# Optimization experiments

Measured on AMD Instinct MI355X. Metric: run time of the kernel, lower is better.

Reference implementation:

```python
import jax, jax.numpy as jnp
import numpy as np

B, S, D, H = 2, 2048, 1024, 16
HD = D // H  # 64
LN_EPS = 1e-5


def setup_inputs() -> dict:
    key = jax.random.key(0)
    ks = jax.random.split(key, 5)
    hidden_states = jax.random.normal(ks[0], (B, S, D), dtype=jnp.float32)
    attention_mask = jnp.zeros((B, 1, 1, S), dtype=jnp.float32)  # additive mask
    # LayerNorm params
    ln_gamma = jnp.ones((D,), dtype=jnp.float32)
    ln_beta = jnp.zeros((D,), dtype=jnp.float32)
    # Q/K/V projections, no bias; stored as [in, out]
    sc = 1.0 / np.sqrt(D)
    Wq = jax.random.normal(ks[1], (D, D), dtype=jnp.float32) * sc
    Wk = jax.random.normal(ks[2], (D, D), dtype=jnp.float32) * sc
    Wv = jax.random.normal(ks[3], (D, D), dtype=jnp.float32) * sc
    return {"hidden_states": hidden_states, "attention_mask": attention_mask,
            "ln_gamma": ln_gamma, "ln_beta": ln_beta, "Wq": Wq, "Wk": Wk, "Wv": Wv}


def _layernorm(x, g, b):
    mu = jnp.mean(x, axis=-1, keepdims=True)
    var = jnp.mean(jnp.square(x - mu), axis=-1, keepdims=True)
    return (x - mu) * jax.lax.rsqrt(var + LN_EPS) * g + b


def reference(hidden_states, attention_mask, ln_gamma, ln_beta, Wq, Wk, Wv):
    h = _layernorm(hidden_states, ln_gamma, ln_beta)          # [B,S,D]
    # project and split heads: [B,S,D] -> [B,H,S,HD]
    def split_heads(x):
        return x.reshape(B, S, H, HD).transpose(0, 2, 1, 3)
    q = split_heads(h @ Wq)
    k = split_heads(h @ Wk)
    v = split_heads(h @ Wv)
    scores = jnp.einsum('bhqd,bhkd->bhqk', q, k) / jnp.sqrt(jnp.float32(HD))
    scores = scores + attention_mask                           # additive mask broadcast
    probs = jax.nn.softmax(scores, axis=-1)                    # dropout p=0 -> identity
    ctx = jnp.einsum('bhqk,bhkd->bhqd', probs, v)              # [B,H,S,HD]
    ctx = ctx.transpose(0, 2, 1, 3).reshape(B, S, H * HD)      # [B,S,D]
    return ctx
```

## Files before the change

kernel.cpp:

```cpp
#include <hip/hip_runtime.h>
#include <hip/hip_bf16.h>
#include <cstdint>

#define B_ 2
#define S_ 2048
#define D_ 1024
#define H_ 16
#define HD_ 64
#define M_ (B_*S_)

#define LOG2E 1.4426950408889634f
#define C1_ (0.125f * LOG2E)

typedef unsigned short u16;
typedef __bf16 bf16x8 __attribute__((ext_vector_type(8)));
typedef u16 u16x8 __attribute__((ext_vector_type(8)));
typedef float f32x4 __attribute__((ext_vector_type(4)));
typedef float f32x16 __attribute__((ext_vector_type(16)));
typedef int i32x4 __attribute__((ext_vector_type(4)));

static __device__ __forceinline__ u16 f2bu(float f) {
  __bf16 b = (__bf16)f;
  return __builtin_bit_cast(unsigned short, b);
}
static __device__ __forceinline__ float bu2f(u16 u) {
  unsigned int v = ((unsigned int)u) << 16;
  return __builtin_bit_cast(float, v);
}

static __device__ __forceinline__ int cvtpk(float a, float b) {
  int r;
  asm("v_cvt_pk_bf16_f32 %0, %1, %2" : "=v"(r) : "v"(a), "v"(b));
  return r;
}
static __device__ __forceinline__ void plswap(int &x, int &y) {
  asm("v_permlane32_swap_b32 %0, %1" : "+v"(x), "+v"(y));
}

#define GLOAD16(g, l) __builtin_amdgcn_global_load_lds( \
    (__attribute__((address_space(1))) void*)(g), \
    (__attribute__((address_space(3))) void*)(l), 16, 0, 0)

__global__ __launch_bounds__(256) void mask_prep(const float* __restrict__ mask,
    float* __restrict__ ms) {
  const int i = blockIdx.x * 256 + threadIdx.x;
  float4 mv = reinterpret_cast<const float4*>(mask)[i];
  float4 sm = {mv.x * LOG2E - 8.0f, mv.y * LOG2E - 8.0f,
               mv.z * LOG2E - 8.0f, mv.w * LOG2E - 8.0f};
  reinterpret_cast<float4*>(ms)[i] = sm;
}

__global__ __launch_bounds__(256) void ln_kernel(const float* __restrict__ x,
    const float* __restrict__ g, const float* __restrict__ be, u16* __restrict__ h) {
  const int row = blockIdx.x;
  const int t = threadIdx.x;
  float4 v = reinterpret_cast<const float4*>(x + (size_t)row * D_)[t];
  float s = v.x + v.y + v.z + v.w;
  float sq = v.x*v.x + v.y*v.y + v.z*v.z + v.w*v.w;
  #pragma unroll
  for (int off = 32; off >= 1; off >>= 1) {
    s  += __shfl_down(s, off);
    sq += __shfl_down(sq, off);
  }
  __shared__ float red[8];
  const int wave = t >> 6, lane = t & 63;
  if (lane == 0) { red[wave] = s; red[4 + wave] = sq; }
  __syncthreads();
  if (t == 0) {
    float ts = red[0]+red[1]+red[2]+red[3];
    float tq = red[4]+red[5]+red[6]+red[7];
    float mu = ts * (1.0f / D_);
    red[0] = mu;
    red[1] = rsqrtf(tq * (1.0f / D_) - mu*mu + 1e-5f);
  }
  __syncthreads();
  const float mu = red[0], rs = red[1];
  float4 gg = reinterpret_cast<const float4*>(g)[t];
  float4 bb = reinterpret_cast<const float4*>(be)[t];
  ushort4 o;
  o.x = f2bu((v.x - mu) * rs * gg.x + bb.x);
  o.y = f2bu((v.y - mu) * rs * gg.y + bb.y);
  o.z = f2bu((v.z - mu) * rs * gg.z + bb.z);
  o.w = f2bu((v.w - mu) * rs * gg.w + bb.w);
  reinterpret_cast<ushort4*>(h + (size_t)row * D_)[t] = o;
}

__global__ __launch_bounds__(256) void wt_kernel(const float* __restrict__ W0,
    const float* __restrict__ W1, const float* __restrict__ W2, u16* __restrict__ wt) {
  const int z = blockIdx.z;
  const float* W = (z == 0) ? W0 : ((z == 1) ? W1 : W2);
  u16* out = wt + (size_t)z * D_ * D_;
  __shared__ float tile[32][33];
  const int n0 = blockIdx.x * 32, k0 = blockIdx.y * 32;
  const int tx = threadIdx.x, ty = threadIdx.y;
  #pragma unroll
  for (int j = 0; j < 4; ++j)
    tile[ty + 8*j][tx] = W[(size_t)(k0 + ty + 8*j) * D_ + n0 + tx];
  __syncthreads();
  #pragma unroll
  for (int j = 0; j < 4; ++j)
    out[(size_t)(n0 + ty + 8*j) * D_ + k0 + tx] = f2bu(tile[tx][ty + 8*j]);
}

__global__ __launch_bounds__(256) void qkv_gemm(const u16* __restrict__ hbuf,
    const u16* __restrict__ wt, u16* __restrict__ qkv) {
  const int z = blockIdx.z;
  const u16* Bt = wt + (size_t)z * D_ * D_;
  u16* outp = qkv + (size_t)z * (B_*H_*S_*HD_);
  __shared__ __align__(16) u16 As[128 * 32];
  __shared__ __align__(16) u16 Bs[128 * 32];
  const int t = threadIdx.x, lane = t & 63, wave = t >> 6;
  const int row0 = blockIdx.y * 128, col0 = blockIdx.x * 128;
  const int wm = wave >> 1, wn = wave & 1;
  f32x4 acc[4][4] = {};
  const int schunk = (t & 3) ^ ((t >> 3) & 3);
  const u16* ag = hbuf + (size_t)(row0 + (t >> 2)) * D_ + schunk * 8;
  const u16* bg = Bt   + (size_t)(col0 + (t >> 2)) * D_ + schunk * 8;
  u16* lA = &As[wave * 512];
  u16* lB = &Bs[wave * 512];
  const char* Ac = (const char*)As;
  const char* Bc = (const char*)Bs;
  const int cbase = (((lane >> 4) ^ ((lane >> 1) & 3)) << 4);

  for (int k0 = 0; k0 < D_; k0 += 32) {
    GLOAD16(ag + k0,           lA);
    GLOAD16(ag + k0 + 64 * D_, lA + 2048);
    GLOAD16(bg + k0,           lB);
    GLOAD16(bg + k0 + 64 * D_, lB + 2048);
    __syncthreads();
    bf16x8 af[4], bfr[4];
    #pragma unroll
    for (int m = 0; m < 4; ++m)
      af[m] = *reinterpret_cast<const bf16x8*>(Ac + (wm*64 + m*16 + (lane & 15)) * 64 + cbase);
    #pragma unroll
    for (int n = 0; n < 4; ++n)
      bfr[n] = *reinterpret_cast<const bf16x8*>(Bc + (wn*64 + n*16 + (lane & 15)) * 64 + cbase);
    #pragma unroll
    for (int m = 0; m < 4; ++m) {
      #pragma unroll
      for (int n = 0; n < 4; ++n)
        acc[m][n] = __builtin_amdgcn_mfma_f32_16x16x32_bf16(af[m], bfr[n], acc[m][n], 0, 0, 0);
    }
    __syncthreads();
  }
  const float scl = (z == 0) ? C1_ : 1.0f;
  #pragma unroll
  for (int m = 0; m < 4; ++m) {
    #pragma unroll
    for (int n = 0; n < 4; ++n) {
      const int gcol = col0 + wn*64 + n*16 + (lane & 15);
      const int hI = gcol >> 6, dI = gcol & 63;
      #pragma unroll
      for (int r = 0; r < 4; ++r) {
        const int grow = row0 + wm*64 + m*16 + (lane >> 4) * 4 + r;
        const int bI = grow >> 11, sI = grow & (S_ - 1);
        size_t idx;
        if (z == 2) idx = ((size_t)(bI * H_ + hI) * HD_ + dI) * S_ + sI;
        else        idx = ((size_t)(bI * H_ + hI) * S_ + sI) * HD_ + dI;
        outp[idx] = f2bu(acc[m][n][r] * scl);
      }
    }
  }
}

static __device__ __forceinline__ void sm_pack(
    const f32x16& s, const float4* __restrict__ mk,
    float& dm, float& lsum, f32x16& o0, f32x16& o1,
    bf16x8& pfA, bf16x8& pfB) {
  float zb[16];
  #pragma unroll
  for (int r = 0; r < 4; ++r) {
    zb[r]      = s[r]      + ((const float*)&mk[0])[r];
    zb[r + 4]  = s[r + 4]  + ((const float*)&mk[1])[r];
    zb[r + 8]  = s[r + 8]  + ((const float*)&mk[2])[r];
    zb[r + 12] = s[r + 12] + ((const float*)&mk[3])[r];
  }
  float a0 = fmaxf(fmaxf(zb[0], zb[1]), zb[2]);
  float a1 = fmaxf(fmaxf(zb[3], zb[4]), zb[5]);
  float a2 = fmaxf(fmaxf(zb[6], zb[7]), zb[8]);
  float a3 = fmaxf(fmaxf(zb[9], zb[10]), zb[11]);
  float a4 = fmaxf(fmaxf(zb[12], zb[13]), zb[14]);
  float tm = fmaxf(fmaxf(fmaxf(a0, a1), fmaxf(a2, a3)), fmaxf(a4, zb[15]));
  if (__builtin_expect(__any(tm > dm + 8.0f), 0)) {
    float tp = fmaxf(tm, __shfl_xor(tm, 32));
    float dnew = fmaxf(dm, tp - 8.0f);
    float sf = __builtin_amdgcn_exp2f(dm - dnew);
    lsum *= sf; o0 = o0 * sf; o1 = o1 * sf; dm = dnew;
  }
  float p[16];
  #pragma unroll
  for (int r = 0; r < 16; ++r) p[r] = __builtin_amdgcn_exp2f(zb[r] - dm);
  float s01 = (p[0] + p[1]) + (p[2] + p[3]);
  float s23 = (p[4] + p[5]) + (p[6] + p[7]);
  float s45 = (p[8] + p[9]) + (p[10] + p[11]);
  float s67 = (p[12] + p[13]) + (p[14] + p[15]);
  lsum += (s01 + s23) + (s45 + s67);
  int pk01 = cvtpk(p[0], p[1]),   pk23 = cvtpk(p[2], p[3]);
  int pk45 = cvtpk(p[4], p[5]),   pk67 = cvtpk(p[6], p[7]);
  int pk89 = cvtpk(p[8], p[9]),   pkAB = cvtpk(p[10], p[11]);
  int pkCD = cvtpk(p[12], p[13]), pkEF = cvtpk(p[14], p[15]);
  plswap(pk01, pk45); plswap(pk23, pk67);
  plswap(pk89, pkCD); plswap(pkAB, pkEF);
  i32x4 c0 = {pk01, pk23, pk45, pk67};
  i32x4 c1 = {pk89, pkAB, pkCD, pkEF};
  pfA = __builtin_bit_cast(bf16x8, c0);
  pfB = __builtin_bit_cast(bf16x8, c1);
}

__global__ __launch_bounds__(256, 3) void attn_kernel(const u16* __restrict__ qkv,
    const float* __restrict__ maskScaled, float* __restrict__ out,
    u16* __restrict__ part1, float* __restrict__ l0a, float* __restrict__ dm0a,
    float* __restrict__ l1a, float* __restrict__ dm1a) {
  const int bid = blockIdx.x;
  const int x = bid & 7, rr = bid >> 3;
  const int w = rr & 31;
  const int pidx = x + ((rr >> 5) << 3);
  const int j = w & 15, g = w >> 4;
  const int hI = pidx & 15, bI = pidx >> 4;
  const size_t plane = (size_t)pidx * (S_ * HD_);
  const u16* Qp  = qkv + plane;
  const u16* Kp  = qkv + (size_t)(B_*H_*S_*HD_) + plane;
  const u16* Vtp = qkv + 2*(size_t)(B_*H_*S_*HD_) + plane;
  const float* maskS = maskScaled + (size_t)bI * S_ + g * 1024;

  const int t = threadIdx.x, lane = t & 63, wave = t >> 6;
  const int cl = lane & 31, hf = lane >> 5;
  const int x7 = cl & 7;
  const int hx16 = (hf ^ x7) << 4;
  const int rg = (cl >> 3) * 1056 + x7 * 128;

  __shared__ __align__(16) u16 KsBuf[2][4224];
  __shared__ __align__(16) u16 VsBuf[2][4224];

  const int q0 = j * 128 + wave * 32;
  bf16x8 qf[4];
  #pragma unroll
  for (int d = 0; d < 4; ++d)
    qf[d] = *reinterpret_cast<const bf16x8*>(
        Qp + (size_t)(q0 + cl) * HD_ + d * 16 + hf * 8);

  const int sr = t >> 3;
  const int scol = ((t & 7) ^ (sr & 7)) << 3;
  const u16* kSrc = Kp  + (size_t)(g * 1024 + sr) * HD_ + scol;
  const u16* vSrc = Vtp + (size_t)sr * S_ + g * 1024 + scol;
  const int dst0 = wave * 528, dst1 = (4 + wave) * 528;

  f32x16 oacc0 = {}, oacc1 = {};
  float dm = 0.f, lsum = 0.f;

  GLOAD16(kSrc,                   &KsBuf[0][dst0]);
  GLOAD16(kSrc + 32 * HD_,        &KsBuf[0][dst1]);
  GLOAD16(vSrc,                   &VsBuf[0][dst0]);
  GLOAD16(vSrc + 32 * (size_t)S_, &VsBuf[0][dst1]);
  int cur = 0;

  for (int kv0 = 0; kv0 < 1024; kv0 += 64) {
    __syncthreads();
    if (kv0 + 64 < 1024) {
      const u16* kn = kSrc + (size_t)(kv0 + 64) * HD_;
      const u16* vn = vSrc + (kv0 + 64);
      GLOAD16(kn,                   &KsBuf[cur ^ 1][dst0]);
      GLOAD16(kn + 32 * HD_,        &KsBuf[cur ^ 1][dst1]);
      GLOAD16(vn,                   &VsBuf[cur ^ 1][dst0]);
      GLOAD16(vn + 32 * (size_t)S_, &VsBuf[cur ^ 1][dst1]);
    }
    const char* Ks = (const char*)KsBuf[cur];
    const char* Vs = (const char*)VsBuf[cur];

    #pragma unroll
    for (int sub = 0; sub < 2; ++sub) {
      const int so = sub * 4224;
      const int vo = sub * 64;
      bf16x8 kf[4];
      #pragma unroll
      for (int d = 0; d < 4; ++d)
        kf[d] = *reinterpret_cast<const bf16x8*>(Ks + so + rg + ((d << 5) ^ hx16));
      f32x16 s = {};
      __builtin_amdgcn_s_setprio(1);
      #pragma unroll
      for (int d = 0; d < 4; ++d)
        s = __builtin_amdgcn_mfma_f32_32x32x16_bf16(kf[d], qf[d], s, 0, 0, 0);
      __builtin_amdgcn_s_setprio(0);
      bf16x8 vf[4];
      vf[0] = *reinterpret_cast<const bf16x8*>(Vs + rg + ((vo + 0) ^ hx16));
      vf[1] = *reinterpret_cast<const bf16x8*>(Vs + rg + 4224 + ((vo + 0) ^ hx16));
      vf[2] = *reinterpret_cast<const bf16x8*>(Vs + rg + ((vo + 32) ^ hx16));
      vf[3] = *reinterpret_cast<const bf16x8*>(Vs + rg + 4224 + ((vo + 32) ^ hx16));
      float4 mk[4];
      #pragma unroll
      for (int i = 0; i < 4; ++i)
        mk[i] = *reinterpret_cast<const float4*>(&maskS[kv0 + sub*32 + 8*i + 4*hf]);
      bf16x8 pA, pB;
      sm_pack(s, mk, dm, lsum, oacc0, oacc1, pA, pB);
      __builtin_amdgcn_s_setprio(1);
      oacc0 = __builtin_amdgcn_mfma_f32_32x32x16_bf16(vf[0], pA, oacc0, 0, 0, 0);
      oacc1 = __builtin_amdgcn_mfma_f32_32x32x16_bf16(vf[1], pA, oacc1, 0, 0, 0);
      oacc0 = __builtin_amdgcn_mfma_f32_32x32x16_bf16(vf[2], pB, oacc0, 0, 0, 0);
      oacc1 = __builtin_amdgcn_mfma_f32_32x32x16_bf16(vf[3], pB, oacc1, 0, 0, 0);
      __builtin_amdgcn_s_setprio(0);
    }
    cur ^= 1;
  }

  lsum += __shfl_xor(lsum, 32);
  const int row = pidx * S_ + q0 + cl;
  if (g == 0) {
    float* orow = out + ((size_t)bI * S_ + q0 + cl) * D_ + hI * HD_;
    #pragma unroll
    for (int jj = 0; jj < 4; ++jj) {
      float4 o0 = {oacc0[4*jj], oacc0[4*jj+1], oacc0[4*jj+2], oacc0[4*jj+3]};
      float4 o1 = {oacc1[4*jj], oacc1[4*jj+1], oacc1[4*jj+2], oacc1[4*jj+3]};
      *reinterpret_cast<float4*>(orow + 8*jj + 4*hf)      = o0;
      *reinterpret_cast<float4*>(orow + 32 + 8*jj + 4*hf) = o1;
    }
    if (hf == 0) { l0a[row] = lsum; dm0a[row] = dm; }
  } else {
    u16* prow = part1 + (size_t)row * HD_;
    #pragma unroll
    for (int jj = 0; jj < 4; ++jj) {
      ushort4 u0 = {f2bu(oacc0[4*jj]), f2bu(oacc0[4*jj+1]), f2bu(oacc0[4*jj+2]), f2bu(oacc0[4*jj+3])};
      ushort4 u1 = {f2bu(oacc1[4*jj]), f2bu(oacc1[4*jj+1]), f2bu(oacc1[4*jj+2]), f2bu(oacc1[4*jj+3])};
      *reinterpret_cast<ushort4*>(prow + 8*jj + 4*hf)      = u0;
      *reinterpret_cast<ushort4*>(prow + 32 + 8*jj + 4*hf) = u1;
    }
    if (hf == 0) { l1a[row] = lsum; dm1a[row] = dm; }
  }
}

__global__ __launch_bounds__(256) void merge_kernel(float* __restrict__ out,
    const u16* __restrict__ part1, const float* __restrict__ l0a,
    const float* __restrict__ dm0a, const float* __restrict__ l1a,
    const float* __restrict__ dm1a) {
  const int e = blockIdx.x * 256 + threadIdx.x;
  const int row = e >> 4;
  const int d4 = (e & 15) << 2;
  const int pidx = row >> 11, q = row & (S_ - 1);
  const int bI = pidx >> 4, hI = pidx & 15;
  const float dm0 = dm0a[row], dm1 = dm1a[row];
  const float dd = fmaxf(dm0, dm1);
  const float f0 = __builtin_amdgcn_exp2f(dm0 - dd);
  const float f1 = __builtin_amdgcn_exp2f(dm1 - dd);
  const float rinv = 1.0f / (l0a[row] * f0 + l1a[row] * f1);
  float* op = out + ((size_t)bI * S_ + q) * D_ + hI * HD_ + d4;
  float4 o0 = *reinterpret_cast<const float4*>(op);
  ushort4 u1 = *reinterpret_cast<const ushort4*>(part1 + (size_t)row * HD_ + d4);
  float4 r;
  r.x = (o0.x * f0 + bu2f(u1.x) * f1) * rinv;
  r.y = (o0.y * f0 + bu2f(u1.y) * f1) * rinv;
  r.z = (o0.z * f0 + bu2f(u1.z) * f1) * rinv;
  r.w = (o0.w * f0 + bu2f(u1.w) * f1) * rinv;
  *reinterpret_cast<float4*>(op) = r;
}

extern "C" void kernel_launch(void* const* d_in, const int* in_sizes, int n_in,
                              void* d_out, int out_size, void* d_ws, size_t ws_size,
                              hipStream_t stream) {
  const float* x     = (const float*)d_in[0];
  const float* mask  = (const float*)d_in[1];
  const float* gamma = (const float*)d_in[2];
  const float* beta  = (const float*)d_in[3];
  const float* Wq    = (const float*)d_in[4];
  const float* Wk    = (const float*)d_in[5];
  const float* Wv    = (const float*)d_in[6];
  float* out = (float*)d_out;

  char* ws = (char*)d_ws;
  u16* hbuf = (u16*)ws;
  char* wtb = ws + (size_t)M_*D_*2;
  u16* wt   = (u16*)wtb;
  u16* qkv  = (u16*)(ws + (size_t)M_*D_*2 + 3ull*D_*D_*2);
  float* maskScaled = (float*)(ws + (size_t)M_*D_*2 + 3ull*D_*D_*2 + 3ull*B_*H_*S_*HD_*2);

  u16* part1 = hbuf;
  float* l0a  = (float*)wtb;
  float* dm0a = (float*)(wtb + (1u<<18));
  float* l1a  = (float*)(wtb + (2u<<18));
  float* dm1a = (float*)(wtb + (3u<<18));

  hipLaunchKernelGGL(mask_prep, dim3(4), dim3(256), 0, stream, mask, maskScaled);
  hipLaunchKernelGGL(ln_kernel, dim3(M_), dim3(256), 0, stream, x, gamma, beta, hbuf);
  hipLaunchKernelGGL(wt_kernel, dim3(32, 32, 3), dim3(32, 8), 0, stream, Wq, Wk, Wv, wt);
  hipLaunchKernelGGL(qkv_gemm, dim3(8, 32, 3), dim3(256), 0, stream, hbuf, wt, qkv);
  hipLaunchKernelGGL(attn_kernel, dim3(1024), dim3(256), 0, stream, qkv, maskScaled,
                     out, part1, l0a, dm0a, l1a, dm1a);
  hipLaunchKernelGGL(merge_kernel, dim3(4096), dim3(256), 0, stream, out, part1,
                     l0a, dm0a, l1a, dm1a);
}
```

Baseline: 119.0 us.

## Single-buffer attention K/V LDS tiles and vectorize V-transpose stores

The attention kernel moves from double-buffered K/V LDS tiles with prefetch of the next tile to a single buffer. The next tile is loaded after a second barrier at the end of each iteration, halving LDS use (likely to raise occupancy) but giving up overlap of global loads with compute. Separately, the QKV projection epilogue writes transposed V as one 4-element vector store instead of four scalar stores. The V path also drops the multiply by scl, which is 1.0 for V, so values are unchanged.

```diff
diff --git a/kernel.cpp b/kernel.cpp
--- a/kernel.cpp
+++ b/kernel.cpp
@@ -150,14 +150,18 @@
     for (int n = 0; n < 4; ++n) {
       const int gcol = col0 + wn*64 + n*16 + (lane & 15);
       const int hI = gcol >> 6, dI = gcol & 63;
-      #pragma unroll
-      for (int r = 0; r < 4; ++r) {
-        const int grow = row0 + wm*64 + m*16 + (lane >> 4) * 4 + r;
-        const int bI = grow >> 11, sI = grow & (S_ - 1);
-        size_t idx;
-        if (z == 2) idx = ((size_t)(bI * H_ + hI) * HD_ + dI) * S_ + sI;
-        else        idx = ((size_t)(bI * H_ + hI) * S_ + sI) * HD_ + dI;
-        outp[idx] = f2bu(acc[m][n][r] * scl);
+      const int grow0 = row0 + wm*64 + m*16 + (lane >> 4) * 4;
+      const int bI = grow0 >> 11, sI0 = grow0 & (S_ - 1);
+      if (z == 2) {
+        ushort4 u = {f2bu(acc[m][n][0]), f2bu(acc[m][n][1]),
+                     f2bu(acc[m][n][2]), f2bu(acc[m][n][3])};
+        *reinterpret_cast<ushort4*>(
+            outp + ((size_t)(bI * H_ + hI) * HD_ + dI) * S_ + sI0) = u;
+      } else {
+        #pragma unroll
+        for (int r = 0; r < 4; ++r)
+          outp[((size_t)(bI * H_ + hI) * S_ + sI0 + r) * HD_ + dI] =
+              f2bu(acc[m][n][r] * scl);
       }
     }
   }
@@ -229,8 +233,8 @@
   const int hx16 = (hf ^ x7) << 4;
   const int rg = (cl >> 3) * 1056 + x7 * 128;
 
-  __shared__ __align__(16) u16 KsBuf[2][4224];
-  __shared__ __align__(16) u16 VsBuf[2][4224];
+  __shared__ __align__(16) u16 Ks_[4224];
+  __shared__ __align__(16) u16 Vs_[4224];
 
   const int q0 = j * 128 + wave * 32;
   bf16x8 qf[4];
@@ -248,24 +252,15 @@
   f32x16 oacc0 = {}, oacc1 = {};
   float dm = 0.f, lsum = 0.f;
 
-  GLOAD16(kSrc,                   &KsBuf[0][dst0]);
-  GLOAD16(kSrc + 32 * HD_,        &KsBuf[0][dst1]);
-  GLOAD16(vSrc,                   &VsBuf[0][dst0]);
-  GLOAD16(vSrc + 32 * (size_t)S_, &VsBuf[0][dst1]);
-  int cur = 0;
+  GLOAD16(kSrc,                   &Ks_[dst0]);
+  GLOAD16(kSrc + 32 * HD_,        &Ks_[dst1]);
+  GLOAD16(vSrc,                   &Vs_[dst0]);
+  GLOAD16(vSrc + 32 * (size_t)S_, &Vs_[dst1]);
 
   for (int kv0 = 0; kv0 < 1024; kv0 += 64) {
     __syncthreads();
-    if (kv0 + 64 < 1024) {
-      const u16* kn = kSrc + (size_t)(kv0 + 64) * HD_;
-      const u16* vn = vSrc + (kv0 + 64);
-      GLOAD16(kn,                   &KsBuf[cur ^ 1][dst0]);
-      GLOAD16(kn + 32 * HD_,        &KsBuf[cur ^ 1][dst1]);
-      GLOAD16(vn,                   &VsBuf[cur ^ 1][dst0]);
-      GLOAD16(vn + 32 * (size_t)S_, &VsBuf[cur ^ 1][dst1]);
-    }
-    const char* Ks = (const char*)KsBuf[cur];
-    const char* Vs = (const char*)VsBuf[cur];
+    const char* Ks = (const char*)Ks_;
+    const char* Vs = (const char*)Vs_;
 
     #pragma unroll
     for (int sub = 0; sub < 2; ++sub) {
@@ -299,7 +294,16 @@
       oacc1 = __builtin_amdgcn_mfma_f32_32x32x16_bf16(vf[3], pB, oacc1, 0, 0, 0);
       __builtin_amdgcn_s_setprio(0);
     }
-    cur ^= 1;
+
+    __syncthreads();
+    if (kv0 + 64 < 1024) {
+      const u16* kn = kSrc + (size_t)(kv0 + 64) * HD_;
+      const u16* vn = vSrc + (kv0 + 64);
+      GLOAD16(kn,                   &Ks_[dst0]);
+      GLOAD16(kn + 32 * HD_,        &Ks_[dst1]);
+      GLOAD16(vn,                   &Vs_[dst0]);
+      GLOAD16(vn + 32 * (size_t)S_, &Vs_[dst1]);
+    }
   }
 
   lsum += __shfl_xor(lsum, 32);
```

New measurement: 112.6 us. -5.4%, faster.
